# Optimization experiments

Measured on AMD Instinct MI355X. Metric: run time of the kernel, lower is better.

## Reference

```python
import jax, jax.numpy as jnp
import numpy as np

HID = 128      # hidden_dim
HEADS = 8      # num_heads
PHD = 16       # per_head_dim
NTYPES = 3     # num_edge_types
N = 50000      # num nodes
E = 250000     # edges per edge type


def setup_inputs() -> dict:
    key = jax.random.key(0)
    ks = jax.random.split(key, 8)
    x = jax.random.normal(ks[0], (N, HID), dtype=jnp.float32)
    adj0 = jax.random.randint(ks[1], (E, 2), 0, N)
    adj1 = jax.random.randint(ks[2], (E, 2), 0, N)
    adj2 = jax.random.randint(ks[3], (E, 2), 0, N)
    # weights stored [in, out] so application is x @ W (same math as torch Linear)
    Wq = jax.random.normal(ks[4], (NTYPES, HID, HEADS * PHD), dtype=jnp.float32) * 0.05
    Wk = jax.random.normal(ks[5], (NTYPES, HID, HEADS * PHD), dtype=jnp.float32) * 0.05
    Wm = jax.random.normal(ks[6], (NTYPES, 2 * HID, HEADS * PHD), dtype=jnp.float32) * 0.05
    bm = jax.random.normal(ks[7], (NTYPES, HEADS * PHD), dtype=jnp.float32) * 0.01
    return {"x": x, "adj0": adj0, "adj1": adj1, "adj2": adj2,
            "Wq": Wq, "Wk": Wk, "Wm": Wm, "bm": bm}


def reference(x, adj0, adj1, adj2, Wq, Wk, Wm, bm):
    scale = PHD ** (-0.5)
    n = x.shape[0]
    msgs, scores, tgts = [], [], []
    for t, adj in enumerate((adj0, adj1, adj2)):
        src_r = x[adj[:, 0]]                       # [E, HID]
        tgt_r = x[adj[:, 1]]                       # [E, HID]
        pair = jnp.concatenate([src_r, tgt_r], axis=1)      # [E, 2*HID]
        m = jax.nn.relu(pair @ Wm[t] + bm[t]).reshape(-1, HEADS, PHD)
        q = (tgt_r @ Wq[t]).reshape(-1, HEADS, PHD) * scale
        k = (src_r @ Wk[t]).reshape(-1, HEADS, PHD)
        s = jnp.einsum('ehd,ehd->eh', q, k)        # [E, HEADS]
        msgs.append(m); scores.append(s); tgts.append(adj[:, 1])
    all_m = jnp.concatenate(msgs, axis=0)          # [TE, HEADS, PHD]
    all_s = jnp.concatenate(scores, axis=0)        # [TE, HEADS]
    all_t = jnp.concatenate(tgts, axis=0)          # [TE]
    # segment log-softmax over edges grouped by target node
    smax = jax.ops.segment_max(all_s, all_t, num_segments=n)        # [N, HEADS]
    shifted = all_s - smax[all_t]
    sumexp = jax.ops.segment_sum(jnp.exp(shifted), all_t, num_segments=n)
    logZ = jnp.log(jnp.where(sumexp > 0, sumexp, 1.0))
    probs = jnp.exp(shifted - logZ[all_t])                          # [TE, HEADS]
    agg = jax.ops.segment_sum(probs[..., None] * all_m, all_t, num_segments=n)
    return agg.reshape(n, HEADS * PHD)
```

## Files before the change

kernel.cpp:

```cpp
#include <hip/hip_runtime.h>

#define HID 128
#define NE 250000
#define NT 3
#define NN 50000
#define NSEG (NT * NN)
#define CAP 24
#define BPAD 136
#define PLANE (NN * 256)
#define GEMM_BLKX 391
#define GEMM_BLOCKS (GEMM_BLKX * 12)
#define EDGE_BLOCKS ((NT * NE + 255) / 256)

typedef unsigned int u32;
typedef unsigned short u16;
typedef __attribute__((ext_vector_type(8))) short short8;
typedef __attribute__((ext_vector_type(4))) float f32x4;

__device__ __forceinline__ u16 f2bf(float f) {
    u32 u = __float_as_uint(f);
    u += 0x7fffu + ((u >> 16) & 1u);
    return (u16)(u >> 16);
}
__device__ __forceinline__ float bflo(u32 u) { return __uint_as_float(u << 16); }
__device__ __forceinline__ float bfhi(u32 u) { return __uint_as_float(u & 0xffff0000u); }

__device__ __forceinline__ short8 pack8(const float4 a, const float4 b) {
    short8 r;
    r[0] = (short)f2bf(a.x); r[1] = (short)f2bf(a.y);
    r[2] = (short)f2bf(a.z); r[3] = (short)f2bf(a.w);
    r[4] = (short)f2bf(b.x); r[5] = (short)f2bf(b.y);
    r[6] = (short)f2bf(b.z); r[7] = (short)f2bf(b.w);
    return r;
}

__global__ __launch_bounds__(256)
void init_kernel(const float* __restrict__ Wq, const float* __restrict__ Wk,
                 const float* __restrict__ Wm,
                 u16* __restrict__ Wtb, u32* __restrict__ counts)
{
    const int b = blockIdx.x, tid = threadIdx.x;
    if (b < 768) {
        const int gid = b * 256 + tid;
        const int mat = gid >> 14;
        const int i   = gid & 16383;
        const int k   = i >> 7;
        const int n   = i & 127;
        const int t   = mat >> 2;
        const int m   = mat & 3;
        const float* src;
        if (m == 0)      src = Wq + (size_t)t * 16384;
        else if (m == 1) src = Wk + (size_t)t * 16384;
        else if (m == 2) src = Wm + (size_t)t * 32768;
        else             src = Wm + (size_t)t * 32768 + 16384;
        Wtb[(size_t)mat * 16384 + n * HID + k] = f2bf(src[i]);
    } else {
        const int gid = (b - 768) * 256 + tid;
        if (gid < NSEG / 4) {
            uint4 z; z.x = 0u; z.y = 0u; z.z = 0u; z.w = 0u;
            ((uint4*)counts)[gid] = z;
        }
    }
}

__global__ __launch_bounds__(256)
void big_kernel(const float* __restrict__ x, const u16* __restrict__ Wtb,
                const float* __restrict__ bm,
                const int* __restrict__ a0, const int* __restrict__ a1,
                const int* __restrict__ a2,
                u32* __restrict__ counts, u16* __restrict__ edata,
                u16* __restrict__ P)
{
    __shared__ u16 Ws[128 * BPAD];
    const int b = blockIdx.x;
    const int tid = threadIdx.x;

    if (b >= GEMM_BLOCKS) {
        const int gid = (b - GEMM_BLOCKS) * 256 + tid;
        if (gid < NT * NE) {
            const int t = gid / NE, e = gid - t * NE;
            const int* adj = (t == 0) ? a0 : (t == 1) ? a1 : a2;
            const int2 pr = ((const int2*)adj)[e];
            const int seg = t * NN + pr.y;
            const u32 pos = atomicAdd(&counts[seg], 1u);
            if (pos < CAP) edata[(size_t)seg * CAP + pos] = (u16)pr.x;
        }
        return;
    }

    const int mat = b % 12;
    const int bx  = b / 12;
    const int t   = mat >> 2, m = mat & 3;
    const u16* Wt = Wtb + (size_t)mat * 16384;

    for (int c = tid; c < 2048; c += 256) {
        const int r = c >> 4, s = (c & 15) * 8;
        *(short8*)&Ws[r * BPAD + s] = *(const short8*)(Wt + r * HID + s);
    }
    __syncthreads();

    const int wave = tid >> 6, lane = tid & 63;
    const int lm = lane & 15, quad = lane >> 4;
    const int r0 = bx * 128 + wave * 32;
    const int ar0 = min(r0 + lm,      NN - 1);
    const int ar1 = min(r0 + 16 + lm, NN - 1);

    f32x4 acc[8][2];
    #pragma unroll
    for (int ct = 0; ct < 8; ++ct) {
        acc[ct][0] = (f32x4){0.f, 0.f, 0.f, 0.f};
        acc[ct][1] = (f32x4){0.f, 0.f, 0.f, 0.f};
    }

    for (int k0 = 0; k0 < HID; k0 += 32) {
        const float* xp0 = x + (size_t)ar0 * HID + k0 + quad * 8;
        const float* xp1 = x + (size_t)ar1 * HID + k0 + quad * 8;
        const short8 X0 = pack8(*(const float4*)xp0, *(const float4*)(xp0 + 4));
        const short8 X1 = pack8(*(const float4*)xp1, *(const float4*)(xp1 + 4));
        #pragma unroll
        for (int ct = 0; ct < 8; ++ct) {
            const short8 Wf = *(const short8*)&Ws[(ct * 16 + lm) * BPAD + k0 + quad * 8];
            acc[ct][0] = __builtin_amdgcn_mfma_f32_16x16x32_bf16(Wf, X0, acc[ct][0], 0, 0, 0);
            acc[ct][1] = __builtin_amdgcn_mfma_f32_16x16x32_bf16(Wf, X1, acc[ct][1], 0, 0, 0);
        }
    }

    const int half = (m == 2 || m == 3) ? 128 : 0;
    const int pidx = (m == 1 || m == 2) ? t : (3 + t);
    u16* Pd = P + (size_t)pidx * PLANE + half;
    const int ocb = quad * 4;
    #pragma unroll
    for (int ct = 0; ct < 8; ++ct) {
        const int oc = ct * 16 + ocb;
        float b0 = 0.f, b1 = 0.f, b2 = 0.f, b3 = 0.f;
        if (m == 3) {
            const float4 bv = *(const float4*)(bm + t * HID + oc);
            b0 = bv.x; b1 = bv.y; b2 = bv.z; b3 = bv.w;
        }
        #pragma unroll
        for (int nt = 0; nt < 2; ++nt) {
            const int node = r0 + nt * 16 + lm;
            if (node < NN) {
                uint2 pk;
                pk.x = (u32)f2bf(acc[ct][nt][0] + b0) | ((u32)f2bf(acc[ct][nt][1] + b1) << 16);
                pk.y = (u32)f2bf(acc[ct][nt][2] + b2) | ((u32)f2bf(acc[ct][nt][3] + b3) << 16);
                *(uint2*)(Pd + (size_t)node * 256 + oc) = pk;
            }
        }
    }
}

__global__ __launch_bounds__(256)
void gather_kernel(const u16* __restrict__ P, const u32* __restrict__ counts,
                   const u16* __restrict__ edata, float* __restrict__ out)
{
    const int wave = threadIdx.x >> 6, lane = threadIdx.x & 63;
    const int node = blockIdx.x * 4 + wave;
    if (node >= NN) return;
    const int j0 = lane * 2;

    int   dgs[NT];
    int   idxs[NT];
    float q0[NT], q1[NT], b0[NT], b1[NT];
    #pragma unroll
    for (int t = 0; t < NT; ++t) {
        const int seg = t * NN + node;
        dgs[t]  = min((int)__builtin_amdgcn_readfirstlane((int)counts[seg]), CAP);
        idxs[t] = (lane < CAP) ? (int)edata[(size_t)seg * CAP + lane] : 0;
        const u16* qb = P + (size_t)(3 + t) * PLANE + (size_t)node * 256;
        const u32 qv = *(const u32*)(qb + j0);
        const u32 bv = *(const u32*)(qb + 128 + j0);
        q0[t] = bflo(qv) * 0.25f;
        q1[t] = bfhi(qv) * 0.25f;
        b0[t] = bflo(bv);
        b1[t] = bfhi(bv);
    }

    float acc0 = 0.f, acc1 = 0.f, den = 0.f;
    #pragma unroll
    for (int t = 0; t < NT; ++t) {
        const int dg = dgs[t];
        const u16* KA = P + (size_t)t * PLANE;
        for (int e = 0; e < dg; e += 8) {
            u32 kv[8], av[8];
            #pragma unroll
            for (int u = 0; u < 8; ++u) {
                int s = __builtin_amdgcn_readlane(idxs[t], e + u);
                s = (e + u < dg) ? s : 0;
                s = __builtin_amdgcn_readfirstlane(s);
                const u16* ka = KA + (size_t)s * 256;
                kv[u] = *(const u32*)(ka + j0);
                av[u] = *(const u32*)(ka + 128 + j0);
            }
            #pragma unroll
            for (int u = 0; u < 8; ++u) {
                float d = q0[t] * bflo(kv[u]) + q1[t] * bfhi(kv[u]);
                d += __shfl_xor(d, 1);
                d += __shfl_xor(d, 2);
                d += __shfl_xor(d, 4);
                float ex = __expf(d);
                ex = (e + u < dg) ? ex : 0.f;
                den  += ex;
                acc0 += ex * fmaxf(bflo(av[u]) + b0[t], 0.f);
                acc1 += ex * fmaxf(bfhi(av[u]) + b1[t], 0.f);
            }
        }
    }

    const float inv = den > 0.f ? 1.f / den : 0.f;
    float2 o;
    o.x = acc0 * inv;
    o.y = acc1 * inv;
    *(float2*)(out + (size_t)node * HID + j0) = o;
}

extern "C" void kernel_launch(void* const* d_in, const int* in_sizes, int n_in,
                              void* d_out, int out_size, void* d_ws, size_t ws_size,
                              hipStream_t stream)
{
    const float* x  = (const float*)d_in[0];
    const int* a0   = (const int*)d_in[1];
    const int* a1   = (const int*)d_in[2];
    const int* a2   = (const int*)d_in[3];
    const float* Wq = (const float*)d_in[4];
    const float* Wk = (const float*)d_in[5];
    const float* Wm = (const float*)d_in[6];
    const float* bm = (const float*)d_in[7];
    float* out = (float*)d_out;

    const size_t planeB = (size_t)PLANE * sizeof(u16);
    char* p = (char*)d_ws;
    u16* P      = (u16*)p;  p += 6 * planeB;
    u16* Wtb    = (u16*)p;  p += 393216;
    u32* counts = (u32*)p;  p += 600000;
    u16* edata  = (u16*)p;

    init_kernel<<<768 + 147, 256, 0, stream>>>(Wq, Wk, Wm, Wtb, counts);
    big_kernel<<<GEMM_BLOCKS + EDGE_BLOCKS, 256, 0, stream>>>(
        x, Wtb, bm, a0, a1, a2, counts, edata, P);
    gather_kernel<<<(NN + 3) / 4, 256, 0, stream>>>(P, counts, edata, out);
}
```

Measured before the change: 271.1 us.

## Merge per-type edge buckets into one per-node list and loop GEMM over matrices

Edge buckets are now one per target node, with the edge type packed into the high bits of a 32-bit entry (CAP 48). The gather loop therefore walks a single list with 12-wide batches instead of three short per-type loops, which cuts loop overhead and idle lanes on low-degree tails. The projection GEMM now uses 391 blocks of 512 threads. Each block loads its x rows once into registers and loops over all 12 weight matrices, restaging each through LDS, instead of re-reading x from global memory for each matrix. The costs are extra __syncthreads per matrix, per-edge selects of the type-specific q and bias, and a larger edge-list buffer.

```diff
diff --git a/kernel.cpp b/kernel.cpp
--- a/kernel.cpp
+++ b/kernel.cpp
@@ -4,13 +4,11 @@
 #define NE 250000
 #define NT 3
 #define NN 50000
-#define NSEG (NT * NN)
-#define CAP 24
+#define CAP 48
 #define BPAD 136
 #define PLANE (NN * 256)
-#define GEMM_BLKX 391
-#define GEMM_BLOCKS (GEMM_BLKX * 12)
-#define EDGE_BLOCKS ((NT * NE + 255) / 256)
+#define GEMM_BLOCKS 391
+#define EDGE_BLOCKS ((NT * NE + 511) / 512)
 
 typedef unsigned int u32;
 typedef unsigned short u16;
@@ -56,19 +54,19 @@
         Wtb[(size_t)mat * 16384 + n * HID + k] = f2bf(src[i]);
     } else {
         const int gid = (b - 768) * 256 + tid;
-        if (gid < NSEG / 4) {
+        if (gid < NN / 4) {
             uint4 z; z.x = 0u; z.y = 0u; z.z = 0u; z.w = 0u;
             ((uint4*)counts)[gid] = z;
         }
     }
 }
 
-__global__ __launch_bounds__(256)
+__global__ __launch_bounds__(512, 4)
 void big_kernel(const float* __restrict__ x, const u16* __restrict__ Wtb,
                 const float* __restrict__ bm,
                 const int* __restrict__ a0, const int* __restrict__ a1,
                 const int* __restrict__ a2,
-                u32* __restrict__ counts, u16* __restrict__ edata,
+                u32* __restrict__ counts, u32* __restrict__ edata,
                 u16* __restrict__ P)
 {
     __shared__ u16 Ws[128 * BPAD];
@@ -76,74 +74,69 @@
     const int tid = threadIdx.x;
 
     if (b >= GEMM_BLOCKS) {
-        const int gid = (b - GEMM_BLOCKS) * 256 + tid;
+        const int gid = (b - GEMM_BLOCKS) * 512 + tid;
         if (gid < NT * NE) {
             const int t = gid / NE, e = gid - t * NE;
             const int* adj = (t == 0) ? a0 : (t == 1) ? a1 : a2;
             const int2 pr = ((const int2*)adj)[e];
-            const int seg = t * NN + pr.y;
-            const u32 pos = atomicAdd(&counts[seg], 1u);
-            if (pos < CAP) edata[(size_t)seg * CAP + pos] = (u16)pr.x;
+            const u32 pos = atomicAdd(&counts[pr.y], 1u);
+            if (pos < CAP)
+                edata[(size_t)pr.y * CAP + pos] = (u32)pr.x | ((u32)t << 16);
         }
         return;
     }
-
-    const int mat = b % 12;
-    const int bx  = b / 12;
-    const int t   = mat >> 2, m = mat & 3;
-    const u16* Wt = Wtb + (size_t)mat * 16384;
-
-    for (int c = tid; c < 2048; c += 256) {
-        const int r = c >> 4, s = (c & 15) * 8;
-        *(short8*)&Ws[r * BPAD + s] = *(const short8*)(Wt + r * HID + s);
-    }
-    __syncthreads();
 
     const int wave = tid >> 6, lane = tid & 63;
     const int lm = lane & 15, quad = lane >> 4;
-    const int r0 = bx * 128 + wave * 32;
-    const int ar0 = min(r0 + lm,      NN - 1);
-    const int ar1 = min(r0 + 16 + lm, NN - 1);
-
-    f32x4 acc[8][2];
+    const int r0 = b * 128 + wave * 16;
+    const int ar = min(r0 + lm, NN - 1);
+    const int node = r0 + lm;
+
+    short8 Xf[4];
     #pragma unroll
-    for (int ct = 0; ct < 8; ++ct) {
-        acc[ct][0] = (f32x4){0.f, 0.f, 0.f, 0.f};
-        acc[ct][1] = (f32x4){0.f, 0.f, 0.f, 0.f};
-    }
-
-    for (int k0 = 0; k0 < HID; k0 += 32) {
-        const float* xp0 = x + (size_t)ar0 * HID + k0 + quad * 8;
-        const float* xp1 = x + (size_t)ar1 * HID + k0 + quad * 8;
-        const short8 X0 = pack8(*(const float4*)xp0, *(const float4*)(xp0 + 4));
-        const short8 X1 = pack8(*(const float4*)xp1, *(const float4*)(xp1 + 4));
-        #pragma unroll
-        for (int ct = 0; ct < 8; ++ct) {
-            const short8 Wf = *(const short8*)&Ws[(ct * 16 + lm) * BPAD + k0 + quad * 8];
-            acc[ct][0] = __builtin_amdgcn_mfma_f32_16x16x32_bf16(Wf, X0, acc[ct][0], 0, 0, 0);
-            acc[ct][1] = __builtin_amdgcn_mfma_f32_16x16x32_bf16(Wf, X1, acc[ct][1], 0, 0, 0);
-        }
-    }
-
-    const int half = (m == 2 || m == 3) ? 128 : 0;
-    const int pidx = (m == 1 || m == 2) ? t : (3 + t);
-    u16* Pd = P + (size_t)pidx * PLANE + half;
-    const int ocb = quad * 4;
-    #pragma unroll
-    for (int ct = 0; ct < 8; ++ct) {
-        const int oc = ct * 16 + ocb;
-        float b0 = 0.f, b1 = 0.f, b2 = 0.f, b3 = 0.f;
-        if (m == 3) {
-            const float4 bv = *(const float4*)(bm + t * HID + oc);
-            b0 = bv.x; b1 = bv.y; b2 = bv.z; b3 = bv.w;
-        }
-        #pragma unroll
-        for (int nt = 0; nt < 2; ++nt) {
-            const int node = r0 + nt * 16 + lm;
-            if (node < NN) {
+    for (int ki = 0; ki < 4; ++ki) {
+        const float* xp = x + (size_t)ar * HID + ki * 32 + quad * 8;
+        Xf[ki] = pack8(*(const float4*)xp, *(const float4*)(xp + 4));
+    }
+
+    for (int mat = 0; mat < 12; ++mat) {
+        const int t = mat >> 2, m = mat & 3;
+        const u16* Wt = Wtb + (size_t)mat * 16384;
+
+        __syncthreads();
+        for (int c = tid; c < 2048; c += 512) {
+            const int r = c >> 4, s = (c & 15) * 8;
+            *(short8*)&Ws[r * BPAD + s] = *(const short8*)(Wt + r * HID + s);
+        }
+        __syncthreads();
+
+        f32x4 acc[8];
+        #pragma unroll
+        for (int ct = 0; ct < 8; ++ct) acc[ct] = (f32x4){0.f, 0.f, 0.f, 0.f};
+        #pragma unroll
+        for (int ki = 0; ki < 4; ++ki) {
+            #pragma unroll
+            for (int ct = 0; ct < 8; ++ct) {
+                const short8 Wf = *(const short8*)&Ws[(ct * 16 + lm) * BPAD + ki * 32 + quad * 8];
+                acc[ct] = __builtin_amdgcn_mfma_f32_16x16x32_bf16(Wf, Xf[ki], acc[ct], 0, 0, 0);
+            }
+        }
+
+        const int half = (m >= 2) ? 128 : 0;
+        const int pidx = (m == 1 || m == 2) ? t : (3 + t);
+        u16* Pd = P + (size_t)pidx * PLANE + half;
+        if (node < NN) {
+            #pragma unroll
+            for (int ct = 0; ct < 8; ++ct) {
+                const int oc = ct * 16 + quad * 4;
+                float b0 = 0.f, b1 = 0.f, b2 = 0.f, b3 = 0.f;
+                if (m == 3) {
+                    const float4 bv = *(const float4*)(bm + t * HID + oc);
+                    b0 = bv.x; b1 = bv.y; b2 = bv.z; b3 = bv.w;
+                }
                 uint2 pk;
-                pk.x = (u32)f2bf(acc[ct][nt][0] + b0) | ((u32)f2bf(acc[ct][nt][1] + b1) << 16);
-                pk.y = (u32)f2bf(acc[ct][nt][2] + b2) | ((u32)f2bf(acc[ct][nt][3] + b3) << 16);
+                pk.x = (u32)f2bf(acc[ct][0] + b0) | ((u32)f2bf(acc[ct][1] + b1) << 16);
+                pk.y = (u32)f2bf(acc[ct][2] + b2) | ((u32)f2bf(acc[ct][3] + b3) << 16);
                 *(uint2*)(Pd + (size_t)node * 256 + oc) = pk;
             }
         }
@@ -152,21 +145,19 @@
 
 __global__ __launch_bounds__(256)
 void gather_kernel(const u16* __restrict__ P, const u32* __restrict__ counts,
-                   const u16* __restrict__ edata, float* __restrict__ out)
+                   const u32* __restrict__ edata, float* __restrict__ out)
 {
     const int wave = threadIdx.x >> 6, lane = threadIdx.x & 63;
     const int node = blockIdx.x * 4 + wave;
     if (node >= NN) return;
     const int j0 = lane * 2;
 
-    int   dgs[NT];
-    int   idxs[NT];
+    const int dg = min((int)__builtin_amdgcn_readfirstlane((int)counts[node]), CAP);
+    const int idxs = (lane < CAP) ? (int)edata[(size_t)node * CAP + lane] : 0;
+
     float q0[NT], q1[NT], b0[NT], b1[NT];
     #pragma unroll
     for (int t = 0; t < NT; ++t) {
-        const int seg = t * NN + node;
-        dgs[t]  = min((int)__builtin_amdgcn_readfirstlane((int)counts[seg]), CAP);
-        idxs[t] = (lane < CAP) ? (int)edata[(size_t)seg * CAP + lane] : 0;
         const u16* qb = P + (size_t)(3 + t) * PLANE + (size_t)node * 256;
         const u32 qv = *(const u32*)(qb + j0);
         const u32 bv = *(const u32*)(qb + 128 + j0);
@@ -177,33 +168,36 @@
     }
 
     float acc0 = 0.f, acc1 = 0.f, den = 0.f;
-    #pragma unroll
-    for (int t = 0; t < NT; ++t) {
-        const int dg = dgs[t];
-        const u16* KA = P + (size_t)t * PLANE;
-        for (int e = 0; e < dg; e += 8) {
-            u32 kv[8], av[8];
-            #pragma unroll
-            for (int u = 0; u < 8; ++u) {
-                int s = __builtin_amdgcn_readlane(idxs[t], e + u);
-                s = (e + u < dg) ? s : 0;
-                s = __builtin_amdgcn_readfirstlane(s);
-                const u16* ka = KA + (size_t)s * 256;
-                kv[u] = *(const u32*)(ka + j0);
-                av[u] = *(const u32*)(ka + 128 + j0);
-            }
-            #pragma unroll
-            for (int u = 0; u < 8; ++u) {
-                float d = q0[t] * bflo(kv[u]) + q1[t] * bfhi(kv[u]);
-                d += __shfl_xor(d, 1);
-                d += __shfl_xor(d, 2);
-                d += __shfl_xor(d, 4);
-                float ex = __expf(d);
-                ex = (e + u < dg) ? ex : 0.f;
-                den  += ex;
-                acc0 += ex * fmaxf(bflo(av[u]) + b0[t], 0.f);
-                acc1 += ex * fmaxf(bfhi(av[u]) + b1[t], 0.f);
-            }
+    for (int e = 0; e < dg; e += 12) {
+        u32 kv[12], av[12];
+        int ty[12];
+        #pragma unroll
+        for (int u = 0; u < 12; ++u) {
+            int w = __builtin_amdgcn_readlane(idxs, e + u);
+            w = (e + u < dg) ? w : 0;
+            w = __builtin_amdgcn_readfirstlane(w);
+            const int tt = w >> 16, s = w & 0xffff;
+            ty[u] = tt;
+            const u16* ka = P + (size_t)tt * PLANE + (size_t)s * 256;
+            kv[u] = *(const u32*)(ka + j0);
+            av[u] = *(const u32*)(ka + 128 + j0);
+        }
+        #pragma unroll
+        for (int u = 0; u < 12; ++u) {
+            const int tt = ty[u];
+            const float cq0 = (tt == 0) ? q0[0] : (tt == 1) ? q0[1] : q0[2];
+            const float cq1 = (tt == 0) ? q1[0] : (tt == 1) ? q1[1] : q1[2];
+            const float cb0 = (tt == 0) ? b0[0] : (tt == 1) ? b0[1] : b0[2];
+            const float cb1 = (tt == 0) ? b1[0] : (tt == 1) ? b1[1] : b1[2];
+            float d = cq0 * bflo(kv[u]) + cq1 * bfhi(kv[u]);
+            d += __shfl_xor(d, 1);
+            d += __shfl_xor(d, 2);
+            d += __shfl_xor(d, 4);
+            float ex = __expf(d);
+            ex = (e + u < dg) ? ex : 0.f;
+            den  += ex;
+            acc0 += ex * fmaxf(bflo(av[u]) + cb0, 0.f);
+            acc1 += ex * fmaxf(bfhi(av[u]) + cb1, 0.f);
         }
     }
 
@@ -232,11 +226,11 @@
     char* p = (char*)d_ws;
     u16* P      = (u16*)p;  p += 6 * planeB;
     u16* Wtb    = (u16*)p;  p += 393216;
-    u32* counts = (u32*)p;  p += 600000;
-    u16* edata  = (u16*)p;
-
-    init_kernel<<<768 + 147, 256, 0, stream>>>(Wq, Wk, Wm, Wtb, counts);
-    big_kernel<<<GEMM_BLOCKS + EDGE_BLOCKS, 256, 0, stream>>>(
+    u32* counts = (u32*)p;  p += 200000;
+    u32* edata  = (u32*)p;
+
+    init_kernel<<<768 + 49, 256, 0, stream>>>(Wq, Wk, Wm, Wtb, counts);
+    big_kernel<<<GEMM_BLOCKS + EDGE_BLOCKS, 512, 0, stream>>>(
         x, Wtb, bm, a0, a1, a2, counts, edata, P);
     gather_kernel<<<(NN + 3) / 4, 256, 0, stream>>>(P, counts, edata, out);
 }
```

Result: faster. 228.3 us (-15.8%).
